# Optimization experiments

Hardware: AMD Instinct MI355X
Metric: run time of the kernel (lower is better)

The kernel has to match this reference:

```python
import jax, jax.numpy as jnp
import numpy as np
import math
from jax import lax

D = 256      # d_model = out_channel
NH = 8       # n_heads
DEP = D // NH
DFF = 1024
B = 48       # conv batch == attended axis in this model
CIN = 32
HW = 32
S = 30 * 30  # (HW-2)**2 after 3x3 valid conv
OUT = 1
FMAX = float(np.finfo(np.float32).max)


def _p(k, shp, scale=0.02):
    return jax.random.normal(k, shp, jnp.float32) * scale


def setup_inputs():
    key = jax.random.key(0)
    ks = jax.random.split(key, 34)
    return {
        'X_en': jax.random.normal(ks[0], (B, CIN, HW, HW), jnp.float32),
        'X_de': jax.random.normal(ks[1], (B, CIN, HW, HW), jnp.float32),
        'conv1_w': _p(ks[2], (D, CIN, 3, 3)), 'conv1_b': _p(ks[3], (D,)),
        'conv2_w': _p(ks[4], (D, D, 3, 3)), 'conv2_b': _p(ks[5], (D,)),
        'enc_wq': _p(ks[6], (D, D)), 'enc_wk': _p(ks[7], (D, D)), 'enc_wv': _p(ks[8], (D, D)),
        'enc_rel_w': _p(ks[9], (S, NH, DEP, B)),
        'enc_ffn_w1': _p(ks[10], (DFF, D)), 'enc_ffn_b1': _p(ks[11], (DFF,)),
        'enc_ffn_w2': _p(ks[12], (D, DFF)), 'enc_ffn_b2': _p(ks[13], (D,)),
        'dec_m_wq': _p(ks[14], (D, D)), 'dec_m_wk': _p(ks[15], (D, D)), 'dec_m_wv': _p(ks[16], (D, D)),
        'dec_m_rel_w': _p(ks[17], (S, NH, DEP, B)),
        'dec_m_lin1_w': _p(ks[18], (B, B)), 'dec_m_lin1_b': _p(ks[19], (B,)),
        'dec_m_lin2_w': _p(ks[20], (B, B)), 'dec_m_lin2_b': _p(ks[21], (B,)),
        'dec_c_wq': _p(ks[22], (D, D)), 'dec_c_wk': _p(ks[23], (D, D)), 'dec_c_wv': _p(ks[24], (D, D)),
        'dec_c_rel_w': _p(ks[25], (S, NH, DEP, B)),
        'dec_ffn_w1': _p(ks[26], (DFF, D)), 'dec_ffn_b1': _p(ks[27], (DFF,)),
        'dec_ffn_w2': _p(ks[28], (D, DFF)), 'dec_ffn_b2': _p(ks[29], (D,)),
        'out_w': _p(ks[30], (OUT, D)), 'out_b': _p(ks[31], (OUT,)),
    }


def _ln(x, eps=1e-5):
    m = jnp.mean(x, -1, keepdims=True)
    v = jnp.mean((x - m) ** 2, -1, keepdims=True)
    return (x - m) / jnp.sqrt(v + eps)


def _skew(q, w):
    # Music-Transformer relative-position skew: matmul + pad + reshape + slice
    emd = jnp.einsum('shbd,shdj->shbj', q, w)  # (S,NH,b,b)
    s, h, i, j = emd.shape
    l = i + j - 1
    x = jnp.concatenate([emd, jnp.zeros_like(emd)], -1).reshape(s, h, -1)
    pad = (-x.shape[-1]) % l
    x = jnp.pad(x, ((0, 0), (0, 0), (0, pad)))
    return x.reshape(s, h, -1, l)[:, :, :i, i - 1:]


def _mha(xq, xk, xv, wq, wk, wv, rel_w, lins=None):
    b, sl, d = xq.shape
    # raw view (not transpose): (b,sl,d) -> (sl,b,NH,DEP), then swap to (sl,NH,b,DEP)
    q = (xq @ wq.T).reshape(sl, b, NH, DEP).swapaxes(1, 2)
    k = (xk @ wk.T).reshape(sl, b, NH, DEP).swapaxes(1, 2)
    v = (xv @ wv.T).reshape(sl, b, NH, DEP).swapaxes(1, 2)
    scores = jnp.einsum('shid,shjd->shij', q, k) / math.sqrt(DEP)  # (sl,NH,b,b)
    if lins is not None:  # masked path: per-call linears + causal mask
        l1w, l1b, l2w, l2b = lins
        qk = scores @ l1w.T + l1b
        qk = jnp.swapaxes(qk, 2, 3) @ l2w.T + l2b
        mask = jnp.triu(jnp.full((b, b), -FMAX, jnp.float32), 1)
        bmm = qk + mask
    else:
        bmm = scores  # linear1/linear2 outputs are discarded when mask=False
    attn = jax.nn.softmax(bmm + _skew(q, rel_w), axis=0)  # softmax over dim 0 (S)
    out = jnp.einsum('shij,shjd->shid', attn, v)  # (sl,NH,b,DEP)
    return out.reshape(b, sl, NH * DEP)  # view(a_s[2], a_s[0], -1)


def reference(X_en, X_de, conv1_w, conv1_b, conv2_w, conv2_b, enc_wq, enc_wk, enc_wv, enc_rel_w, enc_ffn_w1, enc_ffn_b1, enc_ffn_w2, enc_ffn_b2, dec_m_wq, dec_m_wk, dec_m_wv, dec_m_rel_w, dec_m_lin1_w, dec_m_lin1_b, dec_m_lin2_w, dec_m_lin2_b, dec_c_wq, dec_c_wk, dec_c_wv, dec_c_rel_w, dec_ffn_w1, dec_ffn_b1, dec_ffn_w2, dec_ffn_b2, out_w, out_b):
    def conv(x, w, b_, pad):
        y = lax.conv_general_dilated(x, w, (1, 1), [(pad, pad), (pad, pad)],
                                     dimension_numbers=('NCHW', 'OIHW', 'NCHW'))
        return y + b_[None, :, None, None]

    def convs(x):
        return conv(conv(x, conv1_w, conv1_b, 0), conv2_w, conv2_b, 1)

    xpe = convs(X_en)
    xpd = convs(X_de)
    b, d, h, w = xpe.shape
    x_en = xpe.reshape(b, h * w, d)  # raw reshape as in torch source
    x_de = xpd.reshape(b, h * w, d)
    # encoder layer
    a = _mha(x_en, x_en, x_en, enc_wq, enc_wk, enc_wv, enc_rel_w)
    o1 = _ln(x_en + a)
    f = jax.nn.relu(o1 @ enc_ffn_w1.T + enc_ffn_b1) @ enc_ffn_w2.T + enc_ffn_b2
    enc_out = _ln(o1 + f)
    # decoder layer
    m = _mha(x_de, x_de, x_de, dec_m_wq, dec_m_wk, dec_m_wv, dec_m_rel_w,
             (dec_m_lin1_w, dec_m_lin1_b, dec_m_lin2_w, dec_m_lin2_b))
    h1 = _ln(x_de + m)
    c = _mha(h1, enc_out, enc_out, dec_c_wq, dec_c_wk, dec_c_wv, dec_c_rel_w)
    h2 = _ln(c + h1)
    f2 = jax.nn.relu(h2 @ dec_ffn_w1.T + dec_ffn_b1) @ dec_ffn_w2.T + dec_ffn_b2
    h3 = _ln(h2 + f2)
    y = h3 @ out_w.T + out_b
    return jax.nn.softmax(y, axis=0)
```

## Files before the change

kernel.cpp:

```cpp
#include <hip/hip_runtime.h>
#include <float.h>

typedef __bf16 bf16;
typedef __attribute__((ext_vector_type(8))) __bf16 bf16x8;
typedef __attribute__((ext_vector_type(4))) __bf16 bf16x4;
typedef __attribute__((ext_vector_type(4))) float f32x4;

__device__ __forceinline__ int imin(int a, int b) { return a < b ? a : b; }

__device__ __forceinline__ void gl2lds(const bf16* g, bf16* l) {
  __builtin_amdgcn_global_load_lds(
      (const __attribute__((address_space(1))) void*)g,
      (__attribute__((address_space(3))) void*)l, 16, 0, 0);
}

__global__ void k_prep_misc(bf16* zp, const float* __restrict__ l1w,
                            const float* __restrict__ l2w,
                            bf16* __restrict__ L1p, bf16* __restrict__ L2p) {
  zp[threadIdx.x] = (bf16)0.0f;
  for (int i = threadIdx.x; i < 3456; i += 256) {
    int r = i / 72, c = i - r * 72;
    L1p[i] = (c < 48) ? (bf16)l1w[r * 48 + c] : (bf16)0.0f;
    L2p[i] = (c < 48) ? (bf16)l2w[r * 48 + c] : (bf16)0.0f;
  }
}

struct CastSegs { const float* s[13]; bf16* d[13]; int n[13]; };
__global__ void k_cast_all(CastSegs sg, int total) {
  int i = blockIdx.x * 256 + threadIdx.x;
  if (i >= total) return;
  for (int k = 0; k < 13; ++k) {
    if (i < sg.n[k]) { sg.d[k][i] = (bf16)sg.s[k][i]; return; }
    i -= sg.n[k];
  }
}

__global__ __launch_bounds__(256) void k_prep_rel(const float* __restrict__ rel,
                                                  bf16* __restrict__ RelT) {
  __shared__ float tile[32 * 49];
  const int t = threadIdx.x;
  for (int u = 0; u < 8; ++u) {
    const size_t sh = (size_t)blockIdx.x * 8 + u;
    const float* src = rel + sh * 1536;
    bf16* dst = RelT + sh * 1536;
    __syncthreads();
    for (int i = t; i < 1536; i += 256) {
      int k = i / 48, j = i - k * 48;
      tile[k * 49 + j] = src[i];
    }
    __syncthreads();
    for (int i = t; i < 1536; i += 256) {
      int j = i >> 5, k = i & 31;
      dst[i] = (bf16)tile[k * 49 + j];
    }
  }
}

__global__ void k_prep_x(const float* __restrict__ XE, const float* __restrict__ XD,
                         bf16* __restrict__ XR) {
  int idx = blockIdx.x * 256 + threadIdx.x;
  if (idx >= 96 * 1024 * 32) return;
  int b = idx >> 15, r = idx & 32767, pos = r >> 5, ic = r & 31;
  const float* X = (b < 48) ? XE : XD;
  int bl = (b < 48) ? b : b - 48;
  XR[idx] = (bf16)X[((size_t)(bl * 32 + ic) << 10) + pos];
}

__global__ void k_pack_conv(const float* __restrict__ w, bf16* __restrict__ dst,
                            int OC, int IC, int total) {
  int idx = blockIdx.x * 256 + threadIdx.x;
  if (idx >= total) return;
  int t = idx / (OC * IC);
  int rem = idx - t * OC * IC;
  int oc = rem / IC, ic = rem - oc * IC;
  dst[idx] = (bf16)w[(size_t)(oc * IC + ic) * 9 + t];
}

__global__ __launch_bounds__(256, 2) void k_gemm128(
    const bf16* __restrict__ A, const bf16* __restrict__ A2,
    const bf16* __restrict__ B, const bf16* __restrict__ B2, int nsplit,
    const float* __restrict__ bias, bf16* __restrict__ C,
    int M, int N, int K, int relu, int ldc, int coff) {
  __shared__ alignas(16) bf16 SM[16384];
  bf16* As = SM;
  bf16* Asx = SM + 4096;
  bf16* Bs = SM + 8192;
  bf16* Bsx = SM + 12288;
  const int t = threadIdx.x, wave = t >> 6;
  const int lane = t & 63, fr = lane & 15, kq = lane >> 4;
  const int wm = wave & 1, wn = wave >> 1;
  const int m0 = blockIdx.x * 128, n0 = blockIdx.y * 128;
  const int srow = t >> 2, kseg = (t & 3) * 8;
  const bf16* Ause = A; const bf16* Buse = B; int nloc = n0;
  if (n0 >= nsplit) { Ause = A2; Buse = B2; nloc = n0 - nsplit; }
  f32x4 acc[4][4] = {};
  const bf16* gA0 = Ause + (size_t)imin(m0 + srow, M - 1) * K + kseg;
  const bf16* gA1 = Ause + (size_t)imin(m0 + 64 + srow, M - 1) * K + kseg;
  const bf16* gB0 = Buse + (size_t)(nloc + srow) * K + kseg;
  const bf16* gB1 = Buse + (size_t)(nloc + 64 + srow) * K + kseg;
  bf16* sA0 = As + wave * 512;
  bf16* sA1 = As + 2048 + wave * 512;
  bf16* sB0 = Bs + wave * 512;
  bf16* sB1 = Bs + 2048 + wave * 512;
  for (int k0 = 0; k0 < K; k0 += 64) {
    gl2lds(gA0 + k0, sA0);          gl2lds(gA0 + k0 + 32, sA0 + 4096);
    gl2lds(gA1 + k0, sA1);          gl2lds(gA1 + k0 + 32, sA1 + 4096);
    gl2lds(gB0 + k0, sB0);          gl2lds(gB0 + k0 + 32, sB0 + 4096);
    gl2lds(gB1 + k0, sB1);          gl2lds(gB1 + k0 + 32, sB1 + 4096);
    __syncthreads();
    for (int ch = 0; ch < 2; ++ch) {
      const bf16* Ac = ch ? Asx : As;
      const bf16* Bc = ch ? Bsx : Bs;
      bf16x8 af[4], bw[4];
      for (int mt = 0; mt < 4; ++mt)
        af[mt] = *(const bf16x8*)(Ac + (wm * 64 + mt * 16 + fr) * 32 + kq * 8);
      for (int nt = 0; nt < 4; ++nt)
        bw[nt] = *(const bf16x8*)(Bc + (wn * 64 + nt * 16 + fr) * 32 + kq * 8);
      for (int mt = 0; mt < 4; ++mt)
        for (int nt = 0; nt < 4; ++nt)
          acc[mt][nt] = __builtin_amdgcn_mfma_f32_16x16x32_bf16(af[mt], bw[nt], acc[mt][nt], 0, 0, 0);
    }
    __syncthreads();
  }
  bf16* Cst = SM;
  for (int half = 0; half < 2; ++half) {
    if (wm == half) {
      for (int mt = 0; mt < 4; ++mt)
        for (int nt = 0; nt < 4; ++nt) {
          int n = n0 + wn * 64 + nt * 16 + fr;
          float bv = bias ? bias[n] : 0.0f;
          for (int r = 0; r < 4; ++r) {
            float v = acc[mt][nt][r] + bv;
            if (relu) v = fmaxf(v, 0.0f);
            Cst[(mt * 16 + kq * 4 + r) * 128 + wn * 64 + nt * 16 + fr] = (bf16)v;
          }
        }
    }
    __syncthreads();
    for (int i = t; i < 1024; i += 256) {
      int r = i >> 4, cs = i & 15;
      int gm = m0 + half * 64 + r;
      if (gm < M)
        *(bf16x8*)(C + (size_t)gm * ldc + coff + n0 + cs * 8) = *(const bf16x8*)(Cst + r * 128 + cs * 8);
    }
    __syncthreads();
  }
}

template <int CIN, int PAD, int SRCW, int SRCROWS, int CHECK, int TRANS, int MTOT>
__global__ __launch_bounds__(256, 2) void k_conv128(
    const bf16* __restrict__ A, const bf16* __restrict__ Bp,
    const float* __restrict__ bias, bf16* __restrict__ C,
    const bf16* __restrict__ zpage) {
  __shared__ alignas(16) bf16 SM[8192];
  bf16* As = SM;
  bf16* Bs = SM + 4096;
  const int t = threadIdx.x, wave = t >> 6;
  const int lane = t & 63, fr = lane & 15, kq = lane >> 4;
  const int wm = wave & 1, wn = wave >> 1;
  const int m0 = blockIdx.x * 128, n0 = blockIdx.y * 128;
  const int srow = t >> 2, kseg = (t & 3) * 8;
  f32x4 acc[4][4] = {};
  int bb[2], yy[2], xx[2];
  for (int hf = 0; hf < 2; ++hf) {
    int m = imin(m0 + hf * 64 + srow, MTOT - 1);
    int b = m / 900, p = m - b * 900;
    bb[hf] = b; yy[hf] = p / 30; xx[hf] = p - (p / 30) * 30;
  }
  bf16* sA0 = As + wave * 512;
  bf16* sA1 = As + 2048 + wave * 512;
  bf16* sB0 = Bs + wave * 512;
  bf16* sB1 = Bs + 2048 + wave * 512;
  for (int k0 = 0; k0 < CIN; k0 += 32) {
    for (int t9 = 0; t9 < 9; ++t9) {
      const int ky = t9 / 3, kx = t9 - ky * 3;
      const bf16* ga[2];
      for (int hf = 0; hf < 2; ++hf) {
        int sy = yy[hf] + ky - PAD, sx = xx[hf] + kx - PAD;
        bool valid = !CHECK || (sy >= 0 && sy < SRCW && sx >= 0 && sx < SRCW);
        ga[hf] = (valid ? A + (size_t)(bb[hf] * SRCROWS + sy * SRCW + sx) * CIN : zpage) + kseg;
      }
      const bf16* gb = Bp + (size_t)(t9 * 256 + n0 + srow) * CIN + kseg;
      gl2lds(ga[0] + k0, sA0);
      gl2lds(ga[1] + k0, sA1);
      gl2lds(gb + k0, sB0);
      gl2lds(gb + (size_t)64 * CIN + k0, sB1);
      __syncthreads();
      bf16x8 af[4], bw[4];
      for (int mt = 0; mt < 4; ++mt)
        af[mt] = *(const bf16x8*)(As + (wm * 64 + mt * 16 + fr) * 32 + kq * 8);
      for (int nt = 0; nt < 4; ++nt)
        bw[nt] = *(const bf16x8*)(Bs + (wn * 64 + nt * 16 + fr) * 32 + kq * 8);
      for (int mt = 0; mt < 4; ++mt)
        for (int nt = 0; nt < 4; ++nt)
          acc[mt][nt] = __builtin_amdgcn_mfma_f32_16x16x32_bf16(af[mt], bw[nt], acc[mt][nt], 0, 0, 0);
      __syncthreads();
    }
  }
  bf16* Cst = SM;
  for (int half = 0; half < 2; ++half) {
    if (wm == half) {
      for (int mt = 0; mt < 4; ++mt)
        for (int nt = 0; nt < 4; ++nt) {
          int n = n0 + wn * 64 + nt * 16 + fr;
          float bv = bias[n];
          for (int r = 0; r < 4; ++r) {
            float v = acc[mt][nt][r] + bv;
            if (TRANS)
              Cst[(wn * 64 + nt * 16 + fr) * 64 + mt * 16 + kq * 4 + r] = (bf16)v;
            else
              Cst[(mt * 16 + kq * 4 + r) * 128 + wn * 64 + nt * 16 + fr] = (bf16)v;
          }
        }
    }
    __syncthreads();
    if (TRANS) {
      for (int i = t; i < 2048; i += 256) {
        int oc = i >> 4, pc = i & 15;
        int gm = m0 + half * 64 + pc * 4;
        if (gm < MTOT) {
          int b = gm / 900, p = gm - b * 900;
          *(bf16x4*)(C + (size_t)(b * 256 + n0 + oc) * 900 + p) = *(const bf16x4*)(Cst + oc * 64 + pc * 4);
        }
      }
    } else {
      for (int i = t; i < 1024; i += 256) {
        int r = i >> 4, cs = i & 15;
        int gm = m0 + half * 64 + r;
        if (gm < MTOT)
          *(bf16x8*)(C + (size_t)gm * 256 + n0 + cs * 8) = *(const bf16x8*)(Cst + r * 128 + cs * 8);
      }
    }
    __syncthreads();
  }
}

__global__ __launch_bounds__(256, 2) void k_conv2x(
    const bf16* __restrict__ A, const bf16* __restrict__ Bp,
    const float* __restrict__ bias, bf16* __restrict__ C,
    const bf16* __restrict__ zpage) {
  __shared__ alignas(16) bf16 SM[16384];
  bf16* As = SM;
  bf16* Bs = SM + 8192;
  const int t = threadIdx.x, wave = t >> 6;
  const int lane = t & 63, fr = lane & 15, kq = lane >> 4;
  const int wm = wave & 1, wn = wave >> 1;
  const int m0 = blockIdx.x * 128, n0 = blockIdx.y * 128;
  const int srow = t >> 2, kseg = (t & 3) * 8;
  f32x4 acc[4][4] = {};
  int bb[2], yy[2], xx[2];
  for (int hf = 0; hf < 2; ++hf) {
    int m = imin(m0 + hf * 64 + srow, 86399);
    int b = m / 900, p = m - b * 900;
    bb[hf] = b; yy[hf] = p / 30; xx[hf] = p - (p / 30) * 30;
  }
  bf16* sA0 = As + wave * 512;
  bf16* sA1 = As + 2048 + wave * 512;
  bf16* sB0 = Bs + wave * 512;
  bf16* sB1 = Bs + 2048 + wave * 512;
  for (int k0 = 0; k0 < 256; k0 += 64) {
    for (int t9 = 0; t9 < 9; ++t9) {
      const int ky = t9 / 3, kx = t9 - ky * 3;
      const bf16* ga[2];
      for (int hf = 0; hf < 2; ++hf) {
        int sy = yy[hf] + ky - 1, sx = xx[hf] + kx - 1;
        bool valid = (sy >= 0 && sy < 30 && sx >= 0 && sx < 30);
        ga[hf] = (valid ? A + (size_t)(bb[hf] * 900 + sy * 30 + sx) * 256 : zpage) + kseg;
      }
      const bf16* gb = Bp + (size_t)(t9 * 256 + n0 + srow) * 256 + kseg;
      gl2lds(ga[0] + k0, sA0);               gl2lds(ga[0] + k0 + 32, sA0 + 4096);
      gl2lds(ga[1] + k0, sA1);               gl2lds(ga[1] + k0 + 32, sA1 + 4096);
      gl2lds(gb + k0, sB0);                  gl2lds(gb + k0 + 32, sB0 + 4096);
      gl2lds(gb + 64 * 256 + k0, sB1);       gl2lds(gb + 64 * 256 + k0 + 32, sB1 + 4096);
      __syncthreads();
      for (int ch = 0; ch < 2; ++ch) {
        const bf16* Ac = As + ch * 4096;
        const bf16* Bc = Bs + ch * 4096;
        bf16x8 af[4], bw[4];
        for (int mt = 0; mt < 4; ++mt)
          af[mt] = *(const bf16x8*)(Ac + (wm * 64 + mt * 16 + fr) * 32 + kq * 8);
        for (int nt = 0; nt < 4; ++nt)
          bw[nt] = *(const bf16x8*)(Bc + (wn * 64 + nt * 16 + fr) * 32 + kq * 8);
        for (int mt = 0; mt < 4; ++mt)
          for (int nt = 0; nt < 4; ++nt)
            acc[mt][nt] = __builtin_amdgcn_mfma_f32_16x16x32_bf16(af[mt], bw[nt], acc[mt][nt], 0, 0, 0);
      }
      __syncthreads();
    }
  }
  bf16* Cst = SM;
  for (int half = 0; half < 2; ++half) {
    if (wm == half) {
      for (int mt = 0; mt < 4; ++mt)
        for (int nt = 0; nt < 4; ++nt) {
          int n = n0 + wn * 64 + nt * 16 + fr;
          float bv = bias[n];
          for (int r = 0; r < 4; ++r) {
            float v = acc[mt][nt][r] + bv;
            Cst[(wn * 64 + nt * 16 + fr) * 64 + mt * 16 + kq * 4 + r] = (bf16)v;
          }
        }
    }
    __syncthreads();
    for (int i = t; i < 2048; i += 256) {
      int oc = i >> 4, pc = i & 15;
      int gm = m0 + half * 64 + pc * 4;
      int b = gm / 900, p = gm - b * 900;
      *(bf16x4*)(C + (size_t)(b * 256 + n0 + oc) * 900 + p) = *(const bf16x4*)(Cst + oc * 64 + pc * 4);
    }
    __syncthreads();
  }
}

template <int MASKED>
__global__ __launch_bounds__(256, MASKED ? 4 : 5) void k_attn_z(
    const bf16* __restrict__ QKV, const bf16* __restrict__ RelT, bf16* __restrict__ Z,
    const bf16* __restrict__ L1p, const bf16* __restrict__ L2p,
    const float* __restrict__ l1b, const float* __restrict__ l2b) {
  __shared__ alignas(16) bf16 QKs[2][48 * 40];
  __shared__ float EMD[48 * 49];
  __shared__ alignas(16) bf16 zst[48 * 48];
  __shared__ alignas(16) bf16 Sc[MASKED ? 48 * 72 : 8];
  __shared__ alignas(16) bf16 T2b[MASKED ? 48 * 72 : 8];
  const int sh = blockIdx.x, s = sh >> 3, h = sh & 7;
  const int t = threadIdx.x, wave = t >> 6, lane = t & 63, fr = lane & 15, kq = lane >> 4;
  const float scale = 0.17677669529663687f;
  for (int c = t; c < 384; c += 256) {
    int half = c >= 192 ? 1 : 0, cc = c - half * 192;
    int row = cc >> 2, seg = cc & 3;
    *(bf16x8*)(&QKs[half][row * 40 + seg * 8]) =
        *(const bf16x8*)(QKV + (size_t)(s * 48 + row) * 768 + half * 256 + h * 32 + seg * 8);
  }
  if constexpr (MASKED) {
    for (int i = t; i < 768; i += 256) {
      int r = i >> 4, c = 48 + (i & 15);
      Sc[r * 72 + c] = (bf16)0.0f;
      T2b[r * 72 + c] = (bf16)0.0f;
    }
  }
  __syncthreads();
  const bf16* relb = RelT + (size_t)sh * 1536;
  f32x4 sreg[3];
  int u = 0;
  for (int t9 = wave; t9 < 9; t9 += 4, ++u) {
    int ti = t9 / 3, tj = t9 - ti * 3;
    bf16x8 af = *(const bf16x8*)(&QKs[0][(ti * 16 + fr) * 40 + kq * 8]);
    bf16x8 bk = *(const bf16x8*)(&QKs[1][(tj * 16 + fr) * 40 + kq * 8]);
    bf16x8 rf = *(const bf16x8*)(relb + (tj * 16 + fr) * 32 + kq * 8);
    f32x4 sacc = {}, eacc = {};
    sacc = __builtin_amdgcn_mfma_f32_16x16x32_bf16(af, bk, sacc, 0, 0, 0);
    eacc = __builtin_amdgcn_mfma_f32_16x16x32_bf16(af, rf, eacc, 0, 0, 0);
    for (int r = 0; r < 4; ++r)
      EMD[(ti * 16 + kq * 4 + r) * 49 + tj * 16 + fr] = eacc[r];
    if constexpr (MASKED) {
      for (int r = 0; r < 4; ++r)
        Sc[(ti * 16 + kq * 4 + r) * 72 + tj * 16 + fr] = (bf16)(sacc[r] * scale);
    } else {
      for (int r = 0; r < 4; ++r) sreg[u][r] = sacc[r] * scale;
    }
  }
  __syncthreads();
  if constexpr (!MASKED) {
    u = 0;
    for (int t9 = wave; t9 < 9; t9 += 4, ++u) {
      int ti = t9 / 3, tj = t9 - ti * 3;
      for (int r = 0; r < 4; ++r) {
        int i = ti * 16 + kq * 4 + r, j = tj * 16 + fr;
        float v = sreg[u][r];
        if (j <= i) v += EMD[i * 49 + 47 + j - i];
        zst[i * 48 + j] = (bf16)v;
      }
    }
  } else {
    for (int t9 = wave; t9 < 9; t9 += 4) {
      int ti = t9 / 3, tj = t9 - ti * 3;
      f32x4 a2 = {};
      for (int k0 = 0; k0 < 64; k0 += 32) {
        bf16x8 af = *(const bf16x8*)(Sc + (ti * 16 + fr) * 72 + k0 + kq * 8);
        bf16x8 bw = *(const bf16x8*)(L1p + (tj * 16 + fr) * 72 + k0 + kq * 8);
        a2 = __builtin_amdgcn_mfma_f32_16x16x32_bf16(af, bw, a2, 0, 0, 0);
      }
      for (int r = 0; r < 4; ++r) {
        int i = ti * 16 + kq * 4 + r, a = tj * 16 + fr;
        T2b[a * 72 + i] = (bf16)(a2[r] + l1b[a]);
      }
    }
    __syncthreads();
    for (int t9 = wave; t9 < 9; t9 += 4) {
      int ti = t9 / 3, tj = t9 - ti * 3;
      f32x4 a2 = {};
      for (int k0 = 0; k0 < 64; k0 += 32) {
        bf16x8 af = *(const bf16x8*)(T2b + (ti * 16 + fr) * 72 + k0 + kq * 8);
        bf16x8 bw = *(const bf16x8*)(L2p + (tj * 16 + fr) * 72 + k0 + kq * 8);
        a2 = __builtin_amdgcn_mfma_f32_16x16x32_bf16(af, bw, a2, 0, 0, 0);
      }
      for (int r = 0; r < 4; ++r) {
        int aa = ti * 16 + kq * 4 + r, cc = tj * 16 + fr;
        float v;
        if (cc > aa) v = -10000.0f;
        else v = a2[r] + l2b[cc] + EMD[aa * 49 + 47 + cc - aa];
        zst[aa * 48 + cc] = (bf16)v;
      }
    }
  }
  __syncthreads();
  bf16* zb = Z + (size_t)sh * 2304;
  for (int c = t; c < 288; c += 256)
    *(bf16x8*)(zb + c * 8) = *(const bf16x8*)(zst + c * 8);
}

__global__ __launch_bounds__(256) void k_colstats(const bf16* __restrict__ Z,
                                                  float* __restrict__ Mc, float* __restrict__ Ic) {
  __shared__ float rm[32][72], rs[32][72];
  const int t = threadIdx.x, cg = t & 7, sg = t >> 3;
  const bf16* p = Z + blockIdx.x * 64 + cg * 8;
  const int s0 = sg * 29, s1 = imin(900, s0 + 29);
  float m[8], ss[8];
  for (int e = 0; e < 8; ++e) { m[e] = -FLT_MAX; ss[e] = 0.0f; }
  for (int s = s0; s < s1; ++s) {
    bf16x8 zv = *(const bf16x8*)(p + (size_t)s * 18432);
    for (int e = 0; e < 8; ++e) {
      float v = (float)zv[e];
      if (v > m[e]) { ss[e] *= __expf(m[e] - v); m[e] = v; }
      ss[e] += __expf(v - m[e]);
    }
  }
  for (int e = 0; e < 8; ++e) { rm[sg][cg * 8 + e] = m[e]; rs[sg][cg * 8 + e] = ss[e]; }
  __syncthreads();
  if (t < 64) {
    float M2 = -FLT_MAX;
    for (int g = 0; g < 32; ++g) M2 = fmaxf(M2, rm[g][t]);
    float S2 = 0.0f;
    for (int g = 0; g < 32; ++g) S2 += rs[g][t] * __expf(rm[g][t] - M2);
    Mc[blockIdx.x * 64 + t] = M2;
    Ic[blockIdx.x * 64 + t] = 1.0f / S2;
  }
}

__global__ __launch_bounds__(256, 6) void k_attn_av(
    const bf16* __restrict__ Z, const bf16* __restrict__ QKV,
    const float* __restrict__ Mc, const float* __restrict__ Ic, bf16* __restrict__ O) {
  __shared__ alignas(16) bf16 Ps[48 * 72];
  __shared__ alignas(16) bf16 Vt[32 * 72];
  __shared__ alignas(16) bf16 Ost[48 * 32];
  const int sh = blockIdx.x, s = sh >> 3, h = sh & 7;
  const int t = threadIdx.x, wave = t >> 6, lane = t & 63, fr = lane & 15, kq = lane >> 4;
  for (int i = t; i < 768; i += 256) Ps[(i >> 4) * 72 + 48 + (i & 15)] = (bf16)0.0f;
  for (int i = t; i < 512; i += 256) Vt[(i >> 4) * 72 + 48 + (i & 15)] = (bf16)0.0f;
  const bf16* zb = Z + (size_t)sh * 2304;
  const float* mc = Mc + h * 2304;
  const float* ic = Ic + h * 2304;
  for (int c = t; c < 288; c += 256) {
    int r = c / 6, seg = c - r * 6;
    int idx = r * 48 + seg * 8;
    bf16x8 zv = *(const bf16x8*)(zb + idx);
    f32x4 m0v = *(const f32x4*)(mc + idx), m1v = *(const f32x4*)(mc + idx + 4);
    f32x4 i0v = *(const f32x4*)(ic + idx), i1v = *(const f32x4*)(ic + idx + 4);
    bf16x8 pv;
    for (int e = 0; e < 4; ++e) pv[e] = (bf16)(__expf((float)zv[e] - m0v[e]) * i0v[e]);
    for (int e = 0; e < 4; ++e) pv[4 + e] = (bf16)(__expf((float)zv[4 + e] - m1v[e]) * i1v[e]);
    *(bf16x8*)(Ps + r * 72 + seg * 8) = pv;
  }
  for (int c = t; c < 192; c += 256) {
    int j = c >> 2, seg = c & 3;
    bf16x8 v = *(const bf16x8*)(QKV + (size_t)(s * 48 + j) * 768 + 512 + h * 32 + seg * 8);
    for (int e = 0; e < 8; ++e) Vt[(seg * 8 + e) * 72 + j] = v[e];
  }
  __syncthreads();
  for (int t6 = wave; t6 < 6; t6 += 4) {
    int ti = t6 >> 1, td = t6 & 1;
    f32x4 a2 = {};
    for (int k0 = 0; k0 < 64; k0 += 32) {
      bf16x8 af = *(const bf16x8*)(Ps + (ti * 16 + fr) * 72 + k0 + kq * 8);
      bf16x8 bv = *(const bf16x8*)(Vt + (td * 16 + fr) * 72 + k0 + kq * 8);
      a2 = __builtin_amdgcn_mfma_f32_16x16x32_bf16(af, bv, a2, 0, 0, 0);
    }
    for (int r = 0; r < 4; ++r)
      Ost[(ti * 16 + kq * 4 + r) * 32 + td * 16 + fr] = (bf16)a2[r];
  }
  __syncthreads();
  bf16* ob = O + (size_t)sh * 1536;
  for (int c = t; c < 192; c += 256)
    *(bf16x8*)(ob + c * 8) = *(const bf16x8*)(Ost + c * 8);
}

__global__ __launch_bounds__(256) void k_add_ln(
    const bf16* __restrict__ Xa, const bf16* __restrict__ Xb, bf16* __restrict__ out) {
  const int t = threadIdx.x, lane = t & 63, w = t >> 6;
  const size_t off = ((size_t)blockIdx.x * 4 + w) * 256 + lane * 4;
  bf16x4 av = *(const bf16x4*)(Xa + off);
  bf16x4 bv = *(const bf16x4*)(Xb + off);
  f32x4 x;
  for (int c = 0; c < 4; ++c) x[c] = (float)av[c] + (float)bv[c];
  float sum = x[0] + x[1] + x[2] + x[3];
  for (int o = 1; o < 64; o <<= 1) sum += __shfl_xor(sum, o);
  float mean = sum * (1.0f / 256.0f);
  float q = 0.0f;
  for (int c = 0; c < 4; ++c) { float d = x[c] - mean; q += d * d; }
  for (int o = 1; o < 64; o <<= 1) q += __shfl_xor(q, o);
  float rstd = rsqrtf(q * (1.0f / 256.0f) + 1e-5f);
  bf16x4 y;
  for (int c = 0; c < 4; ++c) y[c] = (bf16)((x[c] - mean) * rstd);
  *(bf16x4*)(out + off) = y;
}

__global__ __launch_bounds__(256) void k_ydot(
    const bf16* __restrict__ H, const float* __restrict__ w,
    const float* __restrict__ b, float* __restrict__ Y) {
  const int t = threadIdx.x, lane = t & 63, wv = t >> 6;
  const size_t row = (size_t)blockIdx.x * 4 + wv;
  bf16x4 hx = *(const bf16x4*)(H + row * 256 + lane * 4);
  f32x4 ww = *(const f32x4*)(w + lane * 4);
  float s = (float)hx[0] * ww[0] + (float)hx[1] * ww[1] + (float)hx[2] * ww[2] + (float)hx[3] * ww[3];
  for (int o = 1; o < 64; o <<= 1) s += __shfl_xor(s, o);
  if (lane == 0) Y[row] = s + b[0];
}

__global__ void k_softmax48(const float* __restrict__ Y, float* __restrict__ O) {
  int ss = blockIdx.x * 256 + threadIdx.x;
  if (ss >= 900) return;
  float m = -FLT_MAX;
  for (int b = 0; b < 48; ++b) m = fmaxf(m, Y[b * 900 + ss]);
  float sum = 0.0f;
  for (int b = 0; b < 48; ++b) sum += __expf(Y[b * 900 + ss] - m);
  float inv = 1.0f / sum;
  for (int b = 0; b < 48; ++b) O[b * 900 + ss] = __expf(Y[b * 900 + ss] - m) * inv;
}

extern "C" void kernel_launch(void* const* d_in, const int* in_sizes, int n_in,
                              void* d_out, int out_size, void* d_ws, size_t ws_size,
                              hipStream_t stream) {
  (void)in_sizes; (void)n_in; (void)out_size;
  const float* X_en = (const float*)d_in[0];
  const float* X_de = (const float*)d_in[1];
  const float* conv1_w = (const float*)d_in[2];
  const float* conv1_b = (const float*)d_in[3];
  const float* conv2_w = (const float*)d_in[4];
  const float* conv2_b = (const float*)d_in[5];
  const float* enc_wq = (const float*)d_in[6];
  const float* enc_wk = (const float*)d_in[7];
  const float* enc_wv = (const float*)d_in[8];
  const float* enc_rel = (const float*)d_in[9];
  const float* enc_f1w = (const float*)d_in[10];
  const float* enc_f1b = (const float*)d_in[11];
  const float* enc_f2w = (const float*)d_in[12];
  const float* enc_f2b = (const float*)d_in[13];
  const float* dm_wq = (const float*)d_in[14];
  const float* dm_wk = (const float*)d_in[15];
  const float* dm_wv = (const float*)d_in[16];
  const float* dm_rel = (const float*)d_in[17];
  const float* dm_l1w = (const float*)d_in[18];
  const float* dm_l1b = (const float*)d_in[19];
  const float* dm_l2w = (const float*)d_in[20];
  const float* dm_l2b = (const float*)d_in[21];
  const float* dc_wq = (const float*)d_in[22];
  const float* dc_wk = (const float*)d_in[23];
  const float* dc_wv = (const float*)d_in[24];
  const float* dc_rel = (const float*)d_in[25];
  const float* d_f1w = (const float*)d_in[26];
  const float* d_f1b = (const float*)d_in[27];
  const float* d_f2w = (const float*)d_in[28];
  const float* d_f2b = (const float*)d_in[29];
  const float* out_w = (const float*)d_in[30];
  const float* out_b = (const float*)d_in[31];
  float* OUT = (float*)d_out;

  const size_t SLOT = 22118400;
  char* ws = (char*)d_ws;
  size_t o = 0;
  bf16* S1 = (bf16*)(ws + o); o += SLOT;
  bf16* S2 = (bf16*)(ws + o); o += SLOT;
  bf16* S3 = (bf16*)(ws + o); o += SLOT;
  bf16* S4 = (bf16*)(ws + o); o += SLOT;
  bf16* S5 = (bf16*)(ws + o); o += SLOT;
  char* U = ws + o; o += 33177600 + 3 * SLOT;
  bf16* Zb = (bf16*)U;
  bf16* QKV = (bf16*)(U + 33177600);
  bf16* XR = (bf16*)U;
  bf16* C1R = (bf16*)(U + 12582912);
  bf16* HID = (bf16*)U;
  bf16* wa = (bf16*)(ws + o); o += 4603904 + 16384;
  float* Y = (float*)(ws + o); o += 172800;
  if (ws_size < o) return;

  bf16* zpage = (bf16*)Y;
  float* encM = (float*)S4; float* encI = encM + 18432;
  float* dmM  = (float*)S3; float* dmI  = dmM + 18432;
  float* crM  = (float*)S2; float* crI  = crM + 18432;
  bf16* encRel = S3;
  bf16* dmRel  = S5;
  bf16* crRel  = S3;

  bf16* c1p = wa;
  bf16* c2p = wa + 73728;
  bf16* EQKVw = wa + 663552;
  bf16* MQKVw = wa + 860160;
  bf16* cqw = wa + 1056768;
  bf16* CKVw = wa + 1122304;
  bf16* ef1 = wa + 1253376;
  bf16* ef2 = wa + 1515520;
  bf16* df1 = wa + 1777664;
  bf16* df2 = wa + 2039808;
  bf16* L1p = wa + 2301952;
  bf16* L2p = wa + 2305408;

  auto gemm = [&](const bf16* A, const bf16* B, const float* bias, bf16* C,
                  int M, int N, int K, int relu, int ldc, int coff) {
    k_gemm128<<<dim3((M + 127) / 128, N / 128), dim3(256), 0, stream>>>(
        A, A, B, B, N, bias, C, M, N, K, relu, ldc, coff);
  };

  k_prep_misc<<<dim3(1), dim3(256), 0, stream>>>(zpage, dm_l1w, dm_l2w, L1p, L2p);
  k_pack_conv<<<dim3(288), dim3(256), 0, stream>>>(conv1_w, c1p, 256, 32, 73728);
  k_pack_conv<<<dim3(2304), dim3(256), 0, stream>>>(conv2_w, c2p, 256, 256, 589824);
  {
    CastSegs sg;
    const float* srcs[13] = {enc_wq, enc_wk, enc_wv, dm_wq, dm_wk, dm_wv, dc_wq,
                             dc_wk, dc_wv, enc_f1w, enc_f2w, d_f1w, d_f2w};
    bf16* dsts[13] = {EQKVw, EQKVw + 65536, EQKVw + 131072, MQKVw, MQKVw + 65536,
                      MQKVw + 131072, cqw, CKVw, CKVw + 65536, ef1, ef2, df1, df2};
    int ns[13] = {65536, 65536, 65536, 65536, 65536, 65536, 65536, 65536, 65536,
                  262144, 262144, 262144, 262144};
    int total = 0;
    for (int k = 0; k < 13; ++k) { sg.s[k] = srcs[k]; sg.d[k] = dsts[k]; sg.n[k] = ns[k]; total += ns[k]; }
    k_cast_all<<<dim3((total + 255) / 256), dim3(256), 0, stream>>>(sg, total);
  }

  k_prep_x<<<dim3(12288), dim3(256), 0, stream>>>(X_en, X_de, XR);
  k_conv128<32, 0, 32, 1024, 0, 0, 86400><<<dim3(675, 2), dim3(256), 0, stream>>>(
      XR, c1p, conv1_b, C1R, zpage);
  k_conv2x<<<dim3(675, 2), dim3(256), 0, stream>>>(C1R, c2p, conv2_b, S1, zpage);

  gemm(S1, EQKVw, nullptr, QKV, 43200, 768, 256, 0, 768, 0);
  k_prep_rel<<<dim3(900), dim3(256), 0, stream>>>(enc_rel, encRel);
  k_attn_z<0><<<dim3(7200), dim3(256), 0, stream>>>(QKV, encRel, Zb, nullptr, nullptr, nullptr, nullptr);
  k_colstats<<<dim3(288), dim3(256), 0, stream>>>(Zb, encM, encI);
  k_attn_av<<<dim3(7200), dim3(256), 0, stream>>>(Zb, QKV, encM, encI, S5);
  k_add_ln<<<dim3(10800), dim3(256), 0, stream>>>(S1, S5, S3);
  gemm(S3, ef1, enc_f1b, HID, 43200, 1024, 256, 1, 1024, 0);
  gemm(HID, ef2, enc_f2b, S5, 43200, 256, 1024, 0, 256, 0);
  k_add_ln<<<dim3(10800), dim3(256), 0, stream>>>(S3, S5, S1);

  gemm(S2, MQKVw, nullptr, QKV, 43200, 768, 256, 0, 768, 0);
  k_prep_rel<<<dim3(900), dim3(256), 0, stream>>>(dm_rel, dmRel);
  k_attn_z<1><<<dim3(7200), dim3(256), 0, stream>>>(QKV, dmRel, Zb, L1p, L2p, dm_l1b, dm_l2b);
  k_colstats<<<dim3(288), dim3(256), 0, stream>>>(Zb, dmM, dmI);
  k_attn_av<<<dim3(7200), dim3(256), 0, stream>>>(Zb, QKV, dmM, dmI, S5);
  k_add_ln<<<dim3(10800), dim3(256), 0, stream>>>(S2, S5, S4);

  k_gemm128<<<dim3(338, 6), dim3(256), 0, stream>>>(
      S4, S1, cqw, CKVw, 256, nullptr, QKV, 43200, 768, 256, 0, 768, 0);
  k_prep_rel<<<dim3(900), dim3(256), 0, stream>>>(dc_rel, crRel);
  k_attn_z<0><<<dim3(7200), dim3(256), 0, stream>>>(QKV, crRel, Zb, nullptr, nullptr, nullptr, nullptr);
  k_colstats<<<dim3(288), dim3(256), 0, stream>>>(Zb, crM, crI);
  k_attn_av<<<dim3(7200), dim3(256), 0, stream>>>(Zb, QKV, crM, crI, S5);
  k_add_ln<<<dim3(10800), dim3(256), 0, stream>>>(S5, S4, S3);

  gemm(S3, df1, d_f1b, HID, 43200, 1024, 256, 1, 1024, 0);
  gemm(HID, df2, d_f2b, S5, 43200, 256, 1024, 0, 256, 0);
  k_add_ln<<<dim3(10800), dim3(256), 0, stream>>>(S3, S5, S4);
  k_ydot<<<dim3(10800), dim3(256), 0, stream>>>(S4, out_w, out_b, Y);
  k_softmax48<<<dim3(4), dim3(256), 0, stream>>>(Y, OUT);
}
```

Measured before the change: 1.020 ms.

## Double-buffer LDS with XOR-swizzled layout in GEMM and conv kernels

Both the generic GEMM and the implicit 3x3 conv GEMM now stage tiles into two LDS buffers, so the next K-slice's global-to-LDS loads are issued while MFMAs run on the current one. This removes one barrier per iteration. The LDS tile layout changes from two 32-wide halves to 64-wide rows with an XOR swizzle, meant to cut bank conflicts on fragment reads. LDS use doubles to 64KB per block, which may reduce occupancy under launch_bounds(256,2).

```diff
diff --git a/kernel.cpp b/kernel.cpp
--- a/kernel.cpp
+++ b/kernel.cpp
@@ -81,45 +81,63 @@
     const bf16* __restrict__ B, const bf16* __restrict__ B2, int nsplit,
     const float* __restrict__ bias, bf16* __restrict__ C,
     int M, int N, int K, int relu, int ldc, int coff) {
-  __shared__ alignas(16) bf16 SM[16384];
-  bf16* As = SM;
-  bf16* Asx = SM + 4096;
-  bf16* Bs = SM + 8192;
-  bf16* Bsx = SM + 12288;
+  __shared__ alignas(16) bf16 SM[32768];
   const int t = threadIdx.x, wave = t >> 6;
   const int lane = t & 63, fr = lane & 15, kq = lane >> 4;
   const int wm = wave & 1, wn = wave >> 1;
   const int m0 = blockIdx.x * 128, n0 = blockIdx.y * 128;
-  const int srow = t >> 2, kseg = (t & 3) * 8;
   const bf16* Ause = A; const bf16* Buse = B; int nloc = n0;
   if (n0 >= nsplit) { Ause = A2; Buse = B2; nloc = n0 - nsplit; }
+  const int srow = t >> 3;
+  const int sg8 = (((t & 7) ^ (srow & 7)) << 3);
+  const bf16* gA[4]; const bf16* gB[4];
+#pragma unroll
+  for (int r = 0; r < 4; ++r) {
+    gA[r] = Ause + (size_t)imin(m0 + r * 32 + srow, M - 1) * K + sg8;
+    gB[r] = Buse + (size_t)(nloc + r * 32 + srow) * K + sg8;
+  }
+  const int swz = (kq ^ (fr & 7)) << 3;
+  const int aoff = (wm * 64 + fr) * 64 + swz;
+  const int boff = 8192 + (wn * 64 + fr) * 64 + swz;
   f32x4 acc[4][4] = {};
-  const bf16* gA0 = Ause + (size_t)imin(m0 + srow, M - 1) * K + kseg;
-  const bf16* gA1 = Ause + (size_t)imin(m0 + 64 + srow, M - 1) * K + kseg;
-  const bf16* gB0 = Buse + (size_t)(nloc + srow) * K + kseg;
-  const bf16* gB1 = Buse + (size_t)(nloc + 64 + srow) * K + kseg;
-  bf16* sA0 = As + wave * 512;
-  bf16* sA1 = As + 2048 + wave * 512;
-  bf16* sB0 = Bs + wave * 512;
-  bf16* sB1 = Bs + 2048 + wave * 512;
-  for (int k0 = 0; k0 < K; k0 += 64) {
-    gl2lds(gA0 + k0, sA0);          gl2lds(gA0 + k0 + 32, sA0 + 4096);
-    gl2lds(gA1 + k0, sA1);          gl2lds(gA1 + k0 + 32, sA1 + 4096);
-    gl2lds(gB0 + k0, sB0);          gl2lds(gB0 + k0 + 32, sB0 + 4096);
-    gl2lds(gB1 + k0, sB1);          gl2lds(gB1 + k0 + 32, sB1 + 4096);
-    __syncthreads();
-    for (int ch = 0; ch < 2; ++ch) {
-      const bf16* Ac = ch ? Asx : As;
-      const bf16* Bc = ch ? Bsx : Bs;
-      bf16x8 af[4], bw[4];
-      for (int mt = 0; mt < 4; ++mt)
-        af[mt] = *(const bf16x8*)(Ac + (wm * 64 + mt * 16 + fr) * 32 + kq * 8);
+  const int NU = K >> 6;
+  {
+    bf16* db = SM + wave * 512;
+#pragma unroll
+    for (int r = 0; r < 4; ++r) gl2lds(gA[r], db + r * 2048);
+#pragma unroll
+    for (int r = 0; r < 4; ++r) gl2lds(gB[r], db + 8192 + r * 2048);
+  }
+  __syncthreads();
+  for (int u = 0; u < NU; ++u) {
+    const int cur = u & 1;
+    if (u + 1 < NU) {
+      bf16* db = SM + (cur ^ 1) * 16384 + wave * 512;
+      const int kb = (u + 1) << 6;
+#pragma unroll
+      for (int r = 0; r < 4; ++r) gl2lds(gA[r] + kb, db + r * 2048);
+#pragma unroll
+      for (int r = 0; r < 4; ++r) gl2lds(gB[r] + kb, db + 8192 + r * 2048);
+    }
+    const bf16* buf = SM + cur * 16384;
+    bf16x8 af[2][4], bw[2][4];
+#pragma unroll
+    for (int kk = 0; kk < 2; ++kk) {
+      const int xo = kk << 5;
+#pragma unroll
+      for (int mt = 0; mt < 4; ++mt)
+        af[kk][mt] = *(const bf16x8*)(buf + ((aoff + mt * 1024) ^ xo));
+#pragma unroll
       for (int nt = 0; nt < 4; ++nt)
-        bw[nt] = *(const bf16x8*)(Bc + (wn * 64 + nt * 16 + fr) * 32 + kq * 8);
-      for (int mt = 0; mt < 4; ++mt)
+        bw[kk][nt] = *(const bf16x8*)(buf + ((boff + nt * 1024) ^ xo));
+    }
+#pragma unroll
+    for (int kk = 0; kk < 2; ++kk)
+#pragma unroll
+      for (int mt = 0; mt < 4; ++mt)
+#pragma unroll
         for (int nt = 0; nt < 4; ++nt)
-          acc[mt][nt] = __builtin_amdgcn_mfma_f32_16x16x32_bf16(af[mt], bw[nt], acc[mt][nt], 0, 0, 0);
-    }
+          acc[mt][nt] = __builtin_amdgcn_mfma_f32_16x16x32_bf16(af[kk][mt], bw[kk][nt], acc[mt][nt], 0, 0, 0);
     __syncthreads();
   }
   bf16* Cst = SM;
@@ -239,54 +257,66 @@
     const bf16* __restrict__ A, const bf16* __restrict__ Bp,
     const float* __restrict__ bias, bf16* __restrict__ C,
     const bf16* __restrict__ zpage) {
-  __shared__ alignas(16) bf16 SM[16384];
-  bf16* As = SM;
-  bf16* Bs = SM + 8192;
+  __shared__ alignas(16) bf16 SM[32768];
   const int t = threadIdx.x, wave = t >> 6;
   const int lane = t & 63, fr = lane & 15, kq = lane >> 4;
   const int wm = wave & 1, wn = wave >> 1;
   const int m0 = blockIdx.x * 128, n0 = blockIdx.y * 128;
-  const int srow = t >> 2, kseg = (t & 3) * 8;
+  const int srow = t >> 3;
+  const int sg8 = (((t & 7) ^ (srow & 7)) << 3);
+  int pb[4], py[4], px[4];
+#pragma unroll
+  for (int r = 0; r < 4; ++r) {
+    int m = imin(m0 + r * 32 + srow, 86399);
+    int b = m / 900, p = m - b * 900;
+    pb[r] = b * 900; py[r] = p / 30; px[r] = p - (p / 30) * 30;
+  }
+  const int swz = (kq ^ (fr & 7)) << 3;
+  const int aoff = (wm * 64 + fr) * 64 + swz;
+  const int boff = 8192 + (wn * 64 + fr) * 64 + swz;
   f32x4 acc[4][4] = {};
-  int bb[2], yy[2], xx[2];
-  for (int hf = 0; hf < 2; ++hf) {
-    int m = imin(m0 + hf * 64 + srow, 86399);
-    int b = m / 900, p = m - b * 900;
-    bb[hf] = b; yy[hf] = p / 30; xx[hf] = p - (p / 30) * 30;
-  }
-  bf16* sA0 = As + wave * 512;
-  bf16* sA1 = As + 2048 + wave * 512;
-  bf16* sB0 = Bs + wave * 512;
-  bf16* sB1 = Bs + 2048 + wave * 512;
-  for (int k0 = 0; k0 < 256; k0 += 64) {
-    for (int t9 = 0; t9 < 9; ++t9) {
-      const int ky = t9 / 3, kx = t9 - ky * 3;
-      const bf16* ga[2];
-      for (int hf = 0; hf < 2; ++hf) {
-        int sy = yy[hf] + ky - 1, sx = xx[hf] + kx - 1;
-        bool valid = (sy >= 0 && sy < 30 && sx >= 0 && sx < 30);
-        ga[hf] = (valid ? A + (size_t)(bb[hf] * 900 + sy * 30 + sx) * 256 : zpage) + kseg;
-      }
-      const bf16* gb = Bp + (size_t)(t9 * 256 + n0 + srow) * 256 + kseg;
-      gl2lds(ga[0] + k0, sA0);               gl2lds(ga[0] + k0 + 32, sA0 + 4096);
-      gl2lds(ga[1] + k0, sA1);               gl2lds(ga[1] + k0 + 32, sA1 + 4096);
-      gl2lds(gb + k0, sB0);                  gl2lds(gb + k0 + 32, sB0 + 4096);
-      gl2lds(gb + 64 * 256 + k0, sB1);       gl2lds(gb + 64 * 256 + k0 + 32, sB1 + 4096);
-      __syncthreads();
-      for (int ch = 0; ch < 2; ++ch) {
-        const bf16* Ac = As + ch * 4096;
-        const bf16* Bc = Bs + ch * 4096;
-        bf16x8 af[4], bw[4];
-        for (int mt = 0; mt < 4; ++mt)
-          af[mt] = *(const bf16x8*)(Ac + (wm * 64 + mt * 16 + fr) * 32 + kq * 8);
+  auto stage = [&](int u, int bsel) {
+    const int t9 = u >> 2, k0c = (u & 3) << 6;
+    const int ky = t9 / 3, kx = t9 - ky * 3;
+    bf16* db = SM + bsel * 16384 + wave * 512;
+#pragma unroll
+    for (int r = 0; r < 4; ++r) {
+      int sy = py[r] + ky - 1, sx = px[r] + kx - 1;
+      bool valid = (sy >= 0 && sy < 30 && sx >= 0 && sx < 30);
+      const bf16* g = valid ? (A + (size_t)(pb[r] + sy * 30 + sx) * 256 + k0c + sg8)
+                            : (zpage + sg8);
+      gl2lds(g, db + r * 2048);
+    }
+    const bf16* gb = Bp + (size_t)(t9 * 256 + n0 + srow) * 256 + k0c + sg8;
+#pragma unroll
+    for (int r = 0; r < 4; ++r)
+      gl2lds(gb + (size_t)r * 32 * 256, db + 8192 + r * 2048);
+  };
+  stage(0, 0);
+  __syncthreads();
+  for (int u = 0; u < 36; ++u) {
+    const int cur = u & 1;
+    if (u < 35) stage(u + 1, cur ^ 1);
+    const bf16* buf = SM + cur * 16384;
+    bf16x8 af[2][4], bw[2][4];
+#pragma unroll
+    for (int kk = 0; kk < 2; ++kk) {
+      const int xo = kk << 5;
+#pragma unroll
+      for (int mt = 0; mt < 4; ++mt)
+        af[kk][mt] = *(const bf16x8*)(buf + ((aoff + mt * 1024) ^ xo));
+#pragma unroll
+      for (int nt = 0; nt < 4; ++nt)
+        bw[kk][nt] = *(const bf16x8*)(buf + ((boff + nt * 1024) ^ xo));
+    }
+#pragma unroll
+    for (int kk = 0; kk < 2; ++kk)
+#pragma unroll
+      for (int mt = 0; mt < 4; ++mt)
+#pragma unroll
         for (int nt = 0; nt < 4; ++nt)
-          bw[nt] = *(const bf16x8*)(Bc + (wn * 64 + nt * 16 + fr) * 32 + kq * 8);
-        for (int mt = 0; mt < 4; ++mt)
-          for (int nt = 0; nt < 4; ++nt)
-            acc[mt][nt] = __builtin_amdgcn_mfma_f32_16x16x32_bf16(af[mt], bw[nt], acc[mt][nt], 0, 0, 0);
-      }
-      __syncthreads();
-    }
+          acc[mt][nt] = __builtin_amdgcn_mfma_f32_16x16x32_bf16(af[kk][mt], bw[kk][nt], acc[mt][nt], 0, 0, 0);
+    __syncthreads();
   }
   bf16* Cst = SM;
   for (int half = 0; half < 2; ++half) {
```

New measurement: 1.106 ms. 8.4% more time.
